# Kernel tuning notes

Measured on AMD Instinct MI355X. Metric: run time of the kernel, lower is better.

Reference implementation:

```python
import jax, jax.numpy as jnp
import numpy as np

DIM = 1024
NUM_HEADS = 16
HEAD_DIM = DIM // NUM_HEADS
SCALE = HEAD_DIM ** -0.5


def setup_inputs() -> dict:
    key = jax.random.key(0)
    ks = jax.random.split(key, 9)
    s = 1.0 / np.sqrt(DIM)
    x = jax.random.normal(ks[0], (2, 2048, DIM), dtype=jnp.float32)
    Wq = jax.random.normal(ks[1], (DIM, DIM), dtype=jnp.float32) * s
    Wk = jax.random.normal(ks[2], (DIM, DIM), dtype=jnp.float32) * s
    Wv = jax.random.normal(ks[3], (DIM, DIM), dtype=jnp.float32) * s
    Wp = jax.random.normal(ks[4], (DIM, DIM), dtype=jnp.float32) * s
    bq = jax.random.normal(ks[5], (DIM,), dtype=jnp.float32) * s
    bk = jax.random.normal(ks[6], (DIM,), dtype=jnp.float32) * s
    bv = jax.random.normal(ks[7], (DIM,), dtype=jnp.float32) * s
    bp = jax.random.normal(ks[8], (DIM,), dtype=jnp.float32) * s
    return {"x": x, "Wq": Wq, "bq": bq, "Wk": Wk, "bk": bk,
            "Wv": Wv, "bv": bv, "Wp": Wp, "bp": bp}


def reference(x, Wq, bq, Wk, bk, Wv, bv, Wp, bp):
    B, L, C = x.shape
    H, D = NUM_HEADS, HEAD_DIM
    # Linear projections (torch Linear: x @ W.T + b)
    q = x @ Wq.T + bq
    k = x @ Wk.T + bk
    v = x @ Wv.T + bv
    # (B, L, H*D) -> (B, H, L, D)
    q = q.reshape(B, L, H, D).transpose(0, 2, 1, 3)
    k = k.reshape(B, L, H, D).transpose(0, 2, 1, 3)
    v = v.reshape(B, L, H, D).transpose(0, 2, 1, 3)
    # scaled dot-product attention, full L x L scores (as in source)
    attn = jnp.einsum('bhqd,bhkd->bhqk', q, k) * SCALE
    attn = jax.nn.softmax(attn, axis=-1)
    out = jnp.einsum('bhqk,bhkd->bhqd', attn, v)
    out = out.transpose(0, 2, 1, 3).reshape(B, L, C)
    return out @ Wp.T + bp
```

## Files before the change

kernel.cpp:

```cpp
#include <hip/hip_runtime.h>

#define DIMC 1024
#define SEQL 2048
#define NB   2
#define NH   16
#define HD   64
#define MTOT (NB*SEQL)
#define XSTR 2048
static constexpr float SM_SCALE = 0.125f;
static constexpr float LOG2E    = 1.4426950408889634f;
static constexpr float QSCALE   = SM_SCALE * LOG2E;

typedef short s16x8 __attribute__((ext_vector_type(8)));
typedef short s16x4 __attribute__((ext_vector_type(4)));
typedef float f32x4 __attribute__((ext_vector_type(4)));
typedef int   i32x4 __attribute__((ext_vector_type(4)));

__device__ __forceinline__ unsigned short f2bf(float f) {
    unsigned int u = __float_as_uint(f);
    u += 0x7fffu + ((u >> 16) & 1u);
    return (unsigned short)(u >> 16);
}
__device__ __forceinline__ s16x8 ld8(const unsigned short* p) {
    return *(const s16x8*)p;
}
__device__ __forceinline__ void gld_lds16(const unsigned short* g, unsigned short* l) {
    __builtin_amdgcn_global_load_lds(
        (const __attribute__((address_space(1))) void*)g,
        (__attribute__((address_space(3))) void*)l, 16, 0, 0);
}
__device__ __forceinline__ unsigned int cvtpk(float lo, float hi) {
    unsigned int r;
    asm("v_cvt_pk_bf16_f32 %0, %1, %2" : "=v"(r) : "v"(lo), "v"(hi));
    return r;
}

#define BAR()    asm volatile("s_barrier" ::: "memory")
#define WAITVM4() asm volatile("s_waitcnt vmcnt(4)" ::: "memory")
#define WAITVM0() asm volatile("s_waitcnt vmcnt(0)" ::: "memory")

__global__ __launch_bounds__(256) void cast_all(
    const float* __restrict__ x,
    const float* __restrict__ Wq, const float* __restrict__ Wk,
    const float* __restrict__ Wv, const float* __restrict__ Wp,
    const float* __restrict__ bq, const float* __restrict__ bk,
    const float* __restrict__ bvv,
    unsigned short* __restrict__ xb, unsigned short* __restrict__ wall,
    float* __restrict__ ball)
{
    const int bid = blockIdx.x, tid = threadIdx.x;
    if (bid < 4096) {
        int i = bid * 256 + tid;
        float4 f = ((const float4*)x)[i];
        s16x4 o;
        o[0] = (short)f2bf(f.x); o[1] = (short)f2bf(f.y);
        o[2] = (short)f2bf(f.z); o[3] = (short)f2bf(f.w);
        ((s16x4*)xb)[i] = o;
    } else if (bid < 8192) {
        int j = (bid - 4096) * 256 + tid;
        int r = j >> 18;
        const float* src = (r == 0) ? Wq : (r == 1) ? Wk : (r == 2) ? Wv : Wp;
        float4 f = ((const float4*)src)[j & 262143];
        s16x4 o;
        o[0] = (short)f2bf(f.x); o[1] = (short)f2bf(f.y);
        o[2] = (short)f2bf(f.z); o[3] = (short)f2bf(f.w);
        ((s16x4*)wall)[j] = o;
    } else {
        int t2 = (bid - 8192) * 256 + tid;
        if (t2 < 3072)
            ball[t2] = (t2 < 1024) ? bq[t2]
                     : (t2 < 2048) ? bk[t2 - 1024] : bvv[t2 - 2048];
    }
}

__global__ __launch_bounds__(256) void gemm_tile(
    const unsigned short* __restrict__ A, int astride,
    const unsigned short* __restrict__ Wb,
    const float* __restrict__ bias,
    unsigned short* qk, unsigned short* vtb, float* outf, int mode)
{
    __shared__ __align__(16) unsigned short Asm[128 * 32];
    __shared__ __align__(16) unsigned short Bsm[128 * 32];

    const int t    = threadIdx.x;
    const int lane = t & 63;
    const int l15  = lane & 15;
    const int quad = lane >> 4;
    const int w    = t >> 6;
    const int mrow = (w & 1) * 64;
    const int ncol = (w >> 1) * 64;
    const int nt_total = (int)gridDim.x >> 5;
    const int xcd = blockIdx.x & 7;
    const int i2  = blockIdx.x >> 3;
    const int nt  = xcd * (nt_total >> 3) + (i2 >> 5);
    const int mt  = i2 & 31;
    const int row0 = mt * 128;

    const unsigned short* ga = A  + (size_t)(row0 + (t >> 2)) * astride + (t & 3) * 8;
    const unsigned short* gb = Wb + (size_t)(nt * 128 + (t >> 2)) * DIMC + (t & 3) * 8;
    const size_t gaStep = (size_t)64 * astride;
    const size_t gbStep = (size_t)64 * DIMC;

    f32x4 acc[4][4] = {};

    for (int k0 = 0; k0 < DIMC; k0 += 32) {
        gld_lds16(ga + k0,          Asm + t * 8);
        gld_lds16(ga + gaStep + k0, Asm + 2048 + t * 8);
        gld_lds16(gb + k0,          Bsm + t * 8);
        gld_lds16(gb + gbStep + k0, Bsm + 2048 + t * 8);
        __syncthreads();

        s16x8 a[4], b[4];
#pragma unroll
        for (int mi = 0; mi < 4; ++mi)
            a[mi] = *(const s16x8*)(Asm + (mrow + mi * 16 + l15) * 32 + quad * 8);
#pragma unroll
        for (int ni = 0; ni < 4; ++ni)
            b[ni] = *(const s16x8*)(Bsm + (ncol + ni * 16 + l15) * 32 + quad * 8);
#pragma unroll
        for (int mi = 0; mi < 4; ++mi)
#pragma unroll
            for (int ni = 0; ni < 4; ++ni)
                acc[mi][ni] = __builtin_amdgcn_mfma_f32_16x16x32_bf16(
                    a[mi], b[ni], acc[mi][ni], 0, 0, 0);
        __syncthreads();
    }

    const int proj = nt >> 3;
#pragma unroll
    for (int ni = 0; ni < 4; ++ni) {
        const int cq = (nt & 7) * 128 + ncol + ni * 16 + l15;
        const float bz = bias[proj * 1024 + cq];
#pragma unroll
        for (int mi = 0; mi < 4; ++mi) {
            const int rbase = row0 + mrow + mi * 16 + quad * 4;
            if (mode == 0) {
                if (proj < 2) {
                    const float scale = (proj == 0) ? QSCALE : 1.0f;
#pragma unroll
                    for (int r = 0; r < 4; ++r)
                        qk[(size_t)(rbase + r) * XSTR + proj * DIMC + cq] =
                            f2bf((acc[mi][ni][r] + bz) * scale);
                } else {
                    const int h = cq >> 6, d = cq & 63;
                    const int bb = rbase >> 11, ll = rbase & (SEQL - 1);
                    s16x4 v4;
                    v4[0] = (short)f2bf(acc[mi][ni][0] + bz);
                    v4[1] = (short)f2bf(acc[mi][ni][1] + bz);
                    v4[2] = (short)f2bf(acc[mi][ni][2] + bz);
                    v4[3] = (short)f2bf(acc[mi][ni][3] + bz);
                    *(s16x4*)(vtb + ((size_t)((bb * NH + h) * HD + d)) * SEQL + ll) = v4;
                }
            } else {
#pragma unroll
                for (int r = 0; r < 4; ++r)
                    outf[(size_t)(rbase + r) * DIMC + cq] = acc[mi][ni][r] + bz;
            }
        }
    }
}

__global__ __launch_bounds__(256) void attn_fused(
    unsigned short* xqk,
    const unsigned short* __restrict__ vt)
{
    __shared__ __align__(16) unsigned short Ksm[2][64 * 64];
    __shared__ __align__(16) unsigned short Vsm[2][64 * 64];

    const int t    = threadIdx.x;
    const int lane = t & 63;
    const int l15  = lane & 15;
    const int quad = lane >> 4;
    const int w    = t >> 6;

    const int xcd = blockIdx.x & 7;
    const int ii  = blockIdx.x >> 3;
    const int bh  = (xcd << 2) | (ii >> 4);
    const int qb  = ii & 15;
    const int h  = bh & (NH - 1);
    const int bb = bh >> 4;
    const int q0A = qb * 128 + w * 16;
    const int q0B = q0A + 64;

    unsigned short* qbase = xqk + (size_t)(bb * SEQL) * XSTR + h * HD + quad * 8;
    unsigned short* qrA = qbase + (size_t)(q0A + l15) * XSTR;
    unsigned short* qrB = qbase + (size_t)(q0B + l15) * XSTR;
    const s16x8 bqA0 = ld8(qrA), bqA1 = ld8(qrA + 32);
    const s16x8 bqB0 = ld8(qrB), bqB1 = ld8(qrB + 32);

    s16x8 bones;
#pragma unroll
    for (int e = 0; e < 8; ++e) bones[e] = (short)0x3F80;

    const int tr = t >> 3, tp = t & 7;
    const int swz = (tp ^ (tr & 7)) * 8;
    const unsigned short* kg = xqk + (size_t)bb * SEQL * XSTR + DIMC + h * HD
                               + (size_t)tr * XSTR + swz;
    const unsigned short* vg = vt + (size_t)(bh * HD + tr) * SEQL + swz;

    f32x4 oA[4] = {}, oB[4] = {};
    f32x4 laccA = {}, laccB = {};
    const int xk = l15 & 7;

    auto stage = [&](unsigned short* Kb, unsigned short* Vb, int j) {
#pragma unroll
        for (int g = 0; g < 2; ++g) {
            gld_lds16(kg + (size_t)(j + g * 32) * XSTR, Kb + g * 2048 + t * 8);
            gld_lds16(vg + (size_t)(g * 32) * SEQL + j,  Vb + g * 2048 + t * 8);
        }
    };

    auto compute = [&](const unsigned short* Kc, const unsigned short* Vc) {
#pragma unroll
        for (int hf = 0; hf < 2; ++hf) {
            const int k0 = (hf * 32 + l15) * 64;
            const int k1 = (hf * 32 + 16 + l15) * 64;
            s16x8 a00 = *(const s16x8*)(Kc + k0 + ((quad       ^ xk) * 8));
            s16x8 a01 = *(const s16x8*)(Kc + k0 + (((quad + 4) ^ xk) * 8));
            s16x8 a10 = *(const s16x8*)(Kc + k1 + ((quad       ^ xk) * 8));
            s16x8 a11 = *(const s16x8*)(Kc + k1 + (((quad + 4) ^ xk) * 8));

            s16x8 bv[4];
#pragma unroll
            for (int c = 0; c < 4; ++c) {
                const unsigned short* va = Vc + (c * 16 + l15) * 64 + (quad & 1) * 4;
                const int kc0 = hf * 4 + (quad >> 1);
                s16x4 v0 = *(const s16x4*)(va + ((kc0       ^ xk) * 8));
                s16x4 v1 = *(const s16x4*)(va + (((kc0 + 2) ^ xk) * 8));
                bv[c] = __builtin_shufflevector(v0, v1, 0, 1, 2, 3, 4, 5, 6, 7);
            }

            __builtin_amdgcn_s_setprio(1);
            {
                f32x4 st0 = {}, st1 = {};
                st0 = __builtin_amdgcn_mfma_f32_16x16x32_bf16(a00, bqA0, st0, 0, 0, 0);
                st0 = __builtin_amdgcn_mfma_f32_16x16x32_bf16(a01, bqA1, st0, 0, 0, 0);
                st1 = __builtin_amdgcn_mfma_f32_16x16x32_bf16(a10, bqA0, st1, 0, 0, 0);
                st1 = __builtin_amdgcn_mfma_f32_16x16x32_bf16(a11, bqA1, st1, 0, 0, 0);
                i32x4 api;
                api[0] = (int)cvtpk(__builtin_amdgcn_exp2f(st0[0]),
                                    __builtin_amdgcn_exp2f(st0[1]));
                api[1] = (int)cvtpk(__builtin_amdgcn_exp2f(st0[2]),
                                    __builtin_amdgcn_exp2f(st0[3]));
                api[2] = (int)cvtpk(__builtin_amdgcn_exp2f(st1[0]),
                                    __builtin_amdgcn_exp2f(st1[1]));
                api[3] = (int)cvtpk(__builtin_amdgcn_exp2f(st1[2]),
                                    __builtin_amdgcn_exp2f(st1[3]));
                s16x8 ap = __builtin_bit_cast(s16x8, api);
                laccA = __builtin_amdgcn_mfma_f32_16x16x32_bf16(ap, bones, laccA, 0, 0, 0);
#pragma unroll
                for (int c = 0; c < 4; ++c)
                    oA[c] = __builtin_amdgcn_mfma_f32_16x16x32_bf16(ap, bv[c], oA[c], 0, 0, 0);
            }
            {
                f32x4 st0 = {}, st1 = {};
                st0 = __builtin_amdgcn_mfma_f32_16x16x32_bf16(a00, bqB0, st0, 0, 0, 0);
                st0 = __builtin_amdgcn_mfma_f32_16x16x32_bf16(a01, bqB1, st0, 0, 0, 0);
                st1 = __builtin_amdgcn_mfma_f32_16x16x32_bf16(a10, bqB0, st1, 0, 0, 0);
                st1 = __builtin_amdgcn_mfma_f32_16x16x32_bf16(a11, bqB1, st1, 0, 0, 0);
                i32x4 api;
                api[0] = (int)cvtpk(__builtin_amdgcn_exp2f(st0[0]),
                                    __builtin_amdgcn_exp2f(st0[1]));
                api[1] = (int)cvtpk(__builtin_amdgcn_exp2f(st0[2]),
                                    __builtin_amdgcn_exp2f(st0[3]));
                api[2] = (int)cvtpk(__builtin_amdgcn_exp2f(st1[0]),
                                    __builtin_amdgcn_exp2f(st1[1]));
                api[3] = (int)cvtpk(__builtin_amdgcn_exp2f(st1[2]),
                                    __builtin_amdgcn_exp2f(st1[3]));
                s16x8 ap = __builtin_bit_cast(s16x8, api);
                laccB = __builtin_amdgcn_mfma_f32_16x16x32_bf16(ap, bones, laccB, 0, 0, 0);
#pragma unroll
                for (int c = 0; c < 4; ++c)
                    oB[c] = __builtin_amdgcn_mfma_f32_16x16x32_bf16(ap, bv[c], oB[c], 0, 0, 0);
            }
            __builtin_amdgcn_s_setprio(0);
        }
    };

    stage(Ksm[0], Vsm[0], 0);

#pragma unroll 1
    for (int jt = 0; jt < SEQL / 64; jt += 2) {
        const int j0 = jt * 64;
        stage(Ksm[1], Vsm[1], j0 + 64);
        WAITVM4();
        BAR();
        compute(Ksm[0], Vsm[0]);
        BAR();
        if (jt + 2 < SEQL / 64) {
            stage(Ksm[0], Vsm[0], j0 + 128);
            WAITVM4();
        } else {
            WAITVM0();
        }
        BAR();
        compute(Ksm[1], Vsm[1]);
        BAR();
    }

    float liA[4], liB[4];
#pragma unroll
    for (int r = 0; r < 4; ++r) {
        liA[r] = 1.0f / laccA[r];
        liB[r] = 1.0f / laccB[r];
    }

#pragma unroll
    for (int c = 0; c < 4; ++c) {
        const int d = c * 16 + l15;
#pragma unroll
        for (int r = 0; r < 4; ++r) {
            const int qr = quad * 4 + r;
            xqk[(size_t)(bb * SEQL + q0A + qr) * XSTR + h * HD + d] = f2bf(oA[c][r] * liA[r]);
            xqk[(size_t)(bb * SEQL + q0B + qr) * XSTR + h * HD + d] = f2bf(oB[c][r] * liB[r]);
        }
    }
}

extern "C" void kernel_launch(void* const* d_in, const int* in_sizes, int n_in,
                              void* d_out, int out_size, void* d_ws, size_t ws_size,
                              hipStream_t stream) {
    const float* x  = (const float*)d_in[0];
    const float* Wq = (const float*)d_in[1];
    const float* bq = (const float*)d_in[2];
    const float* Wk = (const float*)d_in[3];
    const float* bk = (const float*)d_in[4];
    const float* Wv = (const float*)d_in[5];
    const float* bv = (const float*)d_in[6];
    const float* Wp = (const float*)d_in[7];
    const float* bp = (const float*)d_in[8];
    float* out = (float*)d_out;
    unsigned short* vtb = (unsigned short*)d_out;
    unsigned short* xqk = (unsigned short*)d_in[0];

    unsigned short* ws   = (unsigned short*)d_ws;
    const size_t XELT = (size_t)MTOT * DIMC;
    const size_t WELT = (size_t)DIMC * DIMC;
    unsigned short* xb   = ws;
    unsigned short* wall = ws + XELT;
    float*          ball = (float*)(ws + 2 * XELT);

    cast_all<<<8204, 256, 0, stream>>>(x, Wq, Wk, Wv, Wp, bq, bk, bv, xb, wall, ball);

    gemm_tile<<<768, 256, 0, stream>>>(xb, DIMC, wall, ball, xqk, vtb, nullptr, 0);

    attn_fused<<<NB * NH * (SEQL / 128), 256, 0, stream>>>(xqk, vtb);

    gemm_tile<<<256, 256, 0, stream>>>(xqk, XSTR, wall + 3 * WELT, bp,
                                       nullptr, nullptr, out, 1);
}
```

Baseline: 214.8 us.

## Double-buffer GEMM LDS tiles to overlap global loads with MFMA

The projection GEMM now keeps two LDS buffers for A and B and prefetches the next K-slice while the current slice is being multiplied. It waits on vmcnt with a bound of four outstanding loads instead of draining all loads before each barrier, and raises wave priority around the MFMA block. The aim is to hide global-to-LDS latency behind matrix work, at the cost of doubled LDS use, which may lower occupancy, and more barriers per iteration.

```diff
diff --git a/kernel.cpp b/kernel.cpp
--- a/kernel.cpp
+++ b/kernel.cpp
@@ -79,8 +79,8 @@
     const float* __restrict__ bias,
     unsigned short* qk, unsigned short* vtb, float* outf, int mode)
 {
-    __shared__ __align__(16) unsigned short Asm[128 * 32];
-    __shared__ __align__(16) unsigned short Bsm[128 * 32];
+    __shared__ __align__(16) unsigned short Asm[2][128 * 32];
+    __shared__ __align__(16) unsigned short Bsm[2][128 * 32];
 
     const int t    = threadIdx.x;
     const int lane = t & 63;
@@ -103,27 +103,49 @@
 
     f32x4 acc[4][4] = {};
 
-    for (int k0 = 0; k0 < DIMC; k0 += 32) {
-        gld_lds16(ga + k0,          Asm + t * 8);
-        gld_lds16(ga + gaStep + k0, Asm + 2048 + t * 8);
-        gld_lds16(gb + k0,          Bsm + t * 8);
-        gld_lds16(gb + gbStep + k0, Bsm + 2048 + t * 8);
-        __syncthreads();
-
+    auto stage = [&](unsigned short* Ab, unsigned short* Bb, int k0) {
+        gld_lds16(ga + k0,          Ab + t * 8);
+        gld_lds16(ga + gaStep + k0, Ab + 2048 + t * 8);
+        gld_lds16(gb + k0,          Bb + t * 8);
+        gld_lds16(gb + gbStep + k0, Bb + 2048 + t * 8);
+    };
+
+    auto compute = [&](const unsigned short* Ac, const unsigned short* Bc) {
         s16x8 a[4], b[4];
 #pragma unroll
         for (int mi = 0; mi < 4; ++mi)
-            a[mi] = *(const s16x8*)(Asm + (mrow + mi * 16 + l15) * 32 + quad * 8);
+            a[mi] = *(const s16x8*)(Ac + (mrow + mi * 16 + l15) * 32 + quad * 8);
 #pragma unroll
         for (int ni = 0; ni < 4; ++ni)
-            b[ni] = *(const s16x8*)(Bsm + (ncol + ni * 16 + l15) * 32 + quad * 8);
+            b[ni] = *(const s16x8*)(Bc + (ncol + ni * 16 + l15) * 32 + quad * 8);
+        __builtin_amdgcn_s_setprio(1);
 #pragma unroll
         for (int mi = 0; mi < 4; ++mi)
 #pragma unroll
             for (int ni = 0; ni < 4; ++ni)
                 acc[mi][ni] = __builtin_amdgcn_mfma_f32_16x16x32_bf16(
                     a[mi], b[ni], acc[mi][ni], 0, 0, 0);
-        __syncthreads();
+        __builtin_amdgcn_s_setprio(0);
+    };
+
+    stage(Asm[0], Bsm[0], 0);
+
+#pragma unroll 1
+    for (int k0 = 0; k0 < DIMC; k0 += 64) {
+        stage(Asm[1], Bsm[1], k0 + 32);
+        WAITVM4();
+        BAR();
+        compute(Asm[0], Bsm[0]);
+        BAR();
+        if (k0 + 64 < DIMC) {
+            stage(Asm[0], Bsm[0], k0 + 64);
+            WAITVM4();
+        } else {
+            WAITVM0();
+        }
+        BAR();
+        compute(Asm[1], Bsm[1]);
+        BAR();
     }
 
     const int proj = nt >> 3;
```

After: 215.3 us. Within noise of the previous version (+0.2%).
